# Kernel tuning notes

Measured on AMD Instinct MI355X. Metric: run time of the kernel, lower is better.

## Reference

```python
import jax, jax.numpy as jnp
import numpy as np

WIND_SIZE = 5
EPSILON = 1e-5
ALPHA = 1.0


def _windows(a, w):
    # a: [B,1,H,W] -> [B, w*w, H, W], zero-padded, window index in (di,dj) row-major
    # order matching torch's unfold(dim=2).unfold(dim=3) + reshape.
    p = w // 2
    B, _, H, W = a.shape
    ap = jnp.pad(a[:, 0], ((0, 0), (p, p), (p, p)))
    taps = [ap[:, i:i + H, j:j + W] for i in range(w) for j in range(w)]
    return jnp.stack(taps, axis=1)


def setup_inputs() -> dict:
    key = jax.random.key(0)
    ks = jax.random.split(key, 6)
    B, H, W = 4, 512, 512
    ww = WIND_SIZE * WIND_SIZE
    fake = jax.random.uniform(ks[0], (B, 1, H, W), dtype=jnp.float32)
    gamma_hdr = jax.random.uniform(ks[1], (B, 1, H, W), dtype=jnp.float32)
    # strictly positive so hdr**(1-f) is well defined
    hdr_original_im = jax.random.uniform(ks[2], (B, 1, H, W), dtype=jnp.float32) + 0.01
    r_weights = jax.random.uniform(ks[3], (B, ww, H, W), dtype=jnp.float32)
    # f_factors in [0.5, 1.5] to avoid division blow-up, realistic gamma factors
    f_factors = jax.random.uniform(ks[4], (B,), dtype=jnp.float32) + 0.5
    hdr_original_gray = jax.random.uniform(ks[5], (B, 1, H, W), dtype=jnp.float32)
    return {
        'fake': fake,
        'gamma_hdr': gamma_hdr,
        'hdr_original_im': hdr_original_im,
        'r_weights': r_weights,
        'f_factors': f_factors,
        'hdr_original_gray': hdr_original_gray,
    }


def reference(fake, gamma_hdr, hdr_original_im, r_weights, f_factors, hdr_original_gray):
    w = WIND_SIZE
    eps = jnp.float32(EPSILON)
    # create_window -> uniform window, normalized: every tap weight = 1/(w*w)
    dist_gauss = jnp.float32(1.0 / (w * w))
    weights_map = dist_gauss * r_weights                      # [B, w*w, H, W]
    weights_map_sum = jnp.sum(weights_map, axis=1, keepdims=True)  # [B,1,H,W]

    def bf_stats(x):
        xw = _windows(x, w)                                   # [B, w*w, H, W]
        mu = jnp.sum(xw * weights_map, axis=1, keepdims=True) / weights_map_sum
        var = jnp.sum((xw - mu) ** 2 * weights_map, axis=1, keepdims=True) / weights_map_sum
        std = jnp.sqrt(jnp.maximum(var, 0.0) + eps)
        return mu, std

    _, std_fake = bf_stats(fake)
    _, std_gamma = bf_stats(gamma_hdr)

    ff = f_factors[:, None, None, None]                       # [B,1,1,1]
    hdr_pow = jnp.power(hdr_original_im, 1.0 - ff)
    hw = _windows(hdr_pow, w)
    hdr_pow_mu = jnp.sum(hw * weights_map, axis=1, keepdims=True) / weights_map_sum

    w_blf = jnp.sum(r_weights, axis=1, keepdims=True) - 1.0   # [B,1,H,W]

    std_objective = (ALPHA / ff) * std_gamma * (hdr_pow_mu + eps)
    gray_max = jnp.max(hdr_original_gray.reshape(hdr_original_gray.shape[0], -1), axis=1)
    std_objective = std_objective * gray_max[:, None, None, None]

    res = 1.0 - std_fake / (std_fake + jax.lax.stop_gradient(std_objective))
    res = res * (w_blf / jnp.mean(w_blf))
    return jnp.mean(res)
```

## Files before the change

### kernel.cpp

```cpp
#include <hip/hip_runtime.h>

#define Bn 4
#define Hn 512
#define Wn 512
#define HWn (Hn * Wn)

constexpr float kEps = 1e-5f;


__global__ __launch_bounds__(256) void gmax_kernel(
    const float* __restrict__ gray, unsigned int* __restrict__ gmax_bits) {
  const int b = blockIdx.y;
  const int i = (blockIdx.x * 256 + threadIdx.x) << 2;
  const float4 g4 = *(const float4*)(gray + b * HWn + i);
  float lmax = fmaxf(fmaxf(g4.x, g4.y), fmaxf(g4.z, g4.w));
#pragma unroll
  for (int off = 32; off > 0; off >>= 1)
    lmax = fmaxf(lmax, __shfl_down(lmax, off));
  __shared__ float smax[4];
  const int lane = threadIdx.x & 63, wid = threadIdx.x >> 6;
  if (lane == 0) smax[wid] = lmax;
  __syncthreads();
  if (threadIdx.x == 0) {
    float m = fmaxf(fmaxf(smax[0], smax[1]), fmaxf(smax[2], smax[3]));
    atomicMax(&gmax_bits[b], __float_as_uint(m));
  }
}

__global__ __launch_bounds__(512, 8) void main_kernel(
    const float* __restrict__ fake, const float* __restrict__ gamma,
    const float* __restrict__ hdr, const float* __restrict__ rw,
    const float* __restrict__ ff, const unsigned int* __restrict__ gmax_bits,
    float* __restrict__ acc) {
  __shared__ float smem[3][6][512];
  __shared__ float sh1[8], sh2[8];

  const int b = blockIdx.x >> 8;
  const int h0 = (blockIdx.x & 255) << 1;
  const float e = 1.0f - ff[b];

  const float* fb = fake + (size_t)b * HWn;
  const float* gb = gamma + (size_t)b * HWn;
  const float* hb = hdr + (size_t)b * HWn;

  float4* smem4 = (float4*)smem;
#pragma unroll
  for (int k = 0; k < 5; ++k) {
    const int i = threadIdx.x + k * 512;
    if (i < 2304) {
      const int a = i / 768;
      const int rem = i - a * 768;
      const int r = rem >> 7;
      const int c4 = rem & 127;
      const int grow = min(max(h0 - 2 + r, 0), Hn - 1);
      const float* src = (a == 0) ? fb : (a == 1) ? gb : hb;
      float4 v = *(const float4*)(src + (grow << 9) + (c4 << 2));
      if (a == 2) {
        v.x = __powf(v.x, e);
        v.y = __powf(v.y, e);
        v.z = __powf(v.z, e);
        v.w = __powf(v.w, e);
      }
      smem4[i] = v;
    }
  }
  __syncthreads();

  const int p = threadIdx.x << 1;
  const int lr = p >> 9;
  const int w0 = p & (Wn - 1);
  const int h = h0 + lr;

  float Sw[2] = {0, 0}, Sf[2] = {0, 0}, Sf2[2] = {0, 0};
  float Sg[2] = {0, 0}, Sg2[2] = {0, 0}, Sh[2] = {0, 0};

  const float* rwb = rw + (size_t)b * 25 * HWn + (h << 9) + w0;

  float cm[6];
#pragma unroll
  for (int i = 0; i < 6; ++i)
    cm[i] = ((unsigned)(w0 - 2 + i) < (unsigned)Wn) ? 1.0f : 0.0f;
  const int c0 = max(w0 - 2, 0);
  const int c2 = min(w0 + 2, Wn - 2);

#pragma unroll
  for (int dyi = 0; dyi < 5; ++dyi) {
    const int r = lr + dyi;
    const float rmask = ((unsigned)(h + dyi - 2) < (unsigned)Hn) ? 1.0f : 0.0f;

    const float2 f0 = *(const float2*)&smem[0][r][c0];
    const float2 f1 = *(const float2*)&smem[0][r][w0];
    const float2 f2 = *(const float2*)&smem[0][r][c2];
    const float2 g0 = *(const float2*)&smem[1][r][c0];
    const float2 g1 = *(const float2*)&smem[1][r][w0];
    const float2 g2 = *(const float2*)&smem[1][r][c2];
    const float2 p0 = *(const float2*)&smem[2][r][c0];
    const float2 p1 = *(const float2*)&smem[2][r][w0];
    const float2 p2 = *(const float2*)&smem[2][r][c2];

    float xf[6] = {f0.x, f0.y, f1.x, f1.y, f2.x, f2.y};
    float xg[6] = {g0.x, g0.y, g1.x, g1.y, g2.x, g2.y};
    float xh[6] = {p0.x, p0.y, p1.x, p1.y, p2.x, p2.y};
#pragma unroll
    for (int i = 0; i < 6; ++i) {
      const float m = rmask * cm[i];
      xf[i] *= m;
      xg[i] *= m;
      xh[i] *= m;
    }
#pragma unroll
    for (int dxi = 0; dxi < 5; ++dxi) {
      const float2 w2 = *(const float2*)(rwb + (size_t)(dyi * 5 + dxi) * HWn);
      const float wk[2] = {w2.x, w2.y};
#pragma unroll
      for (int j = 0; j < 2; ++j) {
        const float w = wk[j];
        const float f = xf[j + dxi], g = xg[j + dxi], hp = xh[j + dxi];
        Sw[j] += w;
        Sf[j] = fmaf(w, f, Sf[j]);
        Sf2[j] = fmaf(w * f, f, Sf2[j]);
        Sg[j] = fmaf(w, g, Sg[j]);
        Sg2[j] = fmaf(w * g, g, Sg2[j]);
        Sh[j] = fmaf(w, hp, Sh[j]);
      }
    }
  }

  const float ffb = ff[b];
  const float gmax = __uint_as_float(gmax_bits[b]);
  float s1 = 0.0f, s2 = 0.0f;
#pragma unroll
  for (int j = 0; j < 2; ++j) {
    const float invSw = 1.0f / Sw[j];
    const float muf = Sf[j] * invSw;
    const float varf = fmaxf(Sf2[j] * invSw - muf * muf, 0.0f);
    const float stdf = sqrtf(varf + kEps);
    const float mug = Sg[j] * invSw;
    const float varg = fmaxf(Sg2[j] * invSw - mug * mug, 0.0f);
    const float stdg = sqrtf(varg + kEps);
    const float hpmu = Sh[j] * invSw;
    const float stdobj = (1.0f / ffb) * stdg * (hpmu + kEps) * gmax;
    const float r = 1.0f - stdf / (stdf + stdobj);
    const float wblf = Sw[j] - 1.0f;
    s1 = fmaf(r, wblf, s1);
    s2 += wblf;
  }
#pragma unroll
  for (int off = 32; off > 0; off >>= 1) {
    s1 += __shfl_down(s1, off);
    s2 += __shfl_down(s2, off);
  }
  const int lane = threadIdx.x & 63, wid = threadIdx.x >> 6;
  if (lane == 0) {
    sh1[wid] = s1;
    sh2[wid] = s2;
  }
  __syncthreads();
  if (threadIdx.x == 0) {
    float a1 = 0.0f, a2 = 0.0f;
#pragma unroll
    for (int i = 0; i < 8; ++i) {
      a1 += sh1[i];
      a2 += sh2[i];
    }
    atomicAdd(&acc[0], a1);
    atomicAdd(&acc[1], a2);
  }
}

__global__ void final_kernel(const float* __restrict__ acc,
                             float* __restrict__ out) {
  if (threadIdx.x == 0) out[0] = acc[0] / acc[1];
}

extern "C" void kernel_launch(void* const* d_in, const int* in_sizes, int n_in,
                              void* d_out, int out_size, void* d_ws,
                              size_t ws_size, hipStream_t stream) {
  const float* fake = (const float*)d_in[0];
  const float* gamma = (const float*)d_in[1];
  const float* hdr = (const float*)d_in[2];
  const float* rw = (const float*)d_in[3];
  const float* ff = (const float*)d_in[4];
  const float* gray = (const float*)d_in[5];
  float* out = (float*)d_out;
  float* ws = (float*)d_ws;
  unsigned int* gmax_bits = (unsigned int*)ws;
  float* acc = ws + 4;

  hipMemsetAsync(d_ws, 0, 64, stream);
  gmax_kernel<<<dim3(HWn / 1024, Bn), 256, 0, stream>>>(gray, gmax_bits);
  main_kernel<<<Bn * Hn / 2, 512, 0, stream>>>(fake, gamma, hdr, rw, ff,
                                               gmax_bits, acc);
  final_kernel<<<1, 64, 0, stream>>>(acc, out);
}
```

Baseline: 195.5 us.

## Process four rows and four pixels per thread with prefetched r_weights

Each block now handles four image rows instead of two and each thread computes four adjacent pixels using float4 loads. This lowers the halo overhead of the shared-memory tile (8 staged rows for 4 output rows instead of 6 for 2). The r_weights for the next window row are prefetched into registers before the shared-memory reads of the current row, to hide global-load latency. In exchange the kernel needs more registers and shared memory per block, and occupancy drops (launch bounds go from 8 to 4).

```diff
diff --git a/kernel.cpp b/kernel.cpp
--- a/kernel.cpp
+++ b/kernel.cpp
@@ -27,95 +27,109 @@
   }
 }
 
-__global__ __launch_bounds__(512, 8) void main_kernel(
+__global__ __launch_bounds__(512, 4) void main_kernel(
     const float* __restrict__ fake, const float* __restrict__ gamma,
     const float* __restrict__ hdr, const float* __restrict__ rw,
     const float* __restrict__ ff, const unsigned int* __restrict__ gmax_bits,
     float* __restrict__ acc) {
-  __shared__ float smem[3][6][512];
+  __shared__ float smem[3][8][512];
   __shared__ float sh1[8], sh2[8];
 
-  const int b = blockIdx.x >> 8;
-  const int h0 = (blockIdx.x & 255) << 1;
+  const int b = blockIdx.x >> 7;
+  const int h0 = (blockIdx.x & 127) << 2;
   const float e = 1.0f - ff[b];
 
   const float* fb = fake + (size_t)b * HWn;
   const float* gb = gamma + (size_t)b * HWn;
   const float* hb = hdr + (size_t)b * HWn;
 
+  const int t = threadIdx.x;
+  const int lr = t >> 7;
+  const int w0 = (t & 127) << 2;
+  const int h = h0 + lr;
+  const float* rwb = rw + (size_t)b * 25 * HWn + (h << 9) + w0;
+
+  float4 wv[5];
+#pragma unroll
+  for (int d = 0; d < 5; ++d)
+    wv[d] = *(const float4*)(rwb + (size_t)d * HWn);
+
   float4* smem4 = (float4*)smem;
 #pragma unroll
-  for (int k = 0; k < 5; ++k) {
-    const int i = threadIdx.x + k * 512;
-    if (i < 2304) {
-      const int a = i / 768;
-      const int rem = i - a * 768;
-      const int r = rem >> 7;
-      const int c4 = rem & 127;
-      const int grow = min(max(h0 - 2 + r, 0), Hn - 1);
-      const float* src = (a == 0) ? fb : (a == 1) ? gb : hb;
-      float4 v = *(const float4*)(src + (grow << 9) + (c4 << 2));
-      if (a == 2) {
-        v.x = __powf(v.x, e);
-        v.y = __powf(v.y, e);
-        v.z = __powf(v.z, e);
-        v.w = __powf(v.w, e);
-      }
-      smem4[i] = v;
-    }
+  for (int k = 0; k < 6; ++k) {
+    const int i = t + (k << 9);
+    const int a = i >> 10;
+    const int rem = i & 1023;
+    const int r = rem >> 7;
+    const int c4 = rem & 127;
+    const int grow = min(max(h0 - 2 + r, 0), Hn - 1);
+    const float* src = (a == 0) ? fb : (a == 1) ? gb : hb;
+    float4 v = *(const float4*)(src + (grow << 9) + (c4 << 2));
+    if (a == 2) {
+      v.x = __powf(v.x, e);
+      v.y = __powf(v.y, e);
+      v.z = __powf(v.z, e);
+      v.w = __powf(v.w, e);
+    }
+    smem4[i] = v;
   }
   __syncthreads();
 
-  const int p = threadIdx.x << 1;
-  const int lr = p >> 9;
-  const int w0 = p & (Wn - 1);
-  const int h = h0 + lr;
-
-  float Sw[2] = {0, 0}, Sf[2] = {0, 0}, Sf2[2] = {0, 0};
-  float Sg[2] = {0, 0}, Sg2[2] = {0, 0}, Sh[2] = {0, 0};
-
-  const float* rwb = rw + (size_t)b * 25 * HWn + (h << 9) + w0;
-
-  float cm[6];
-#pragma unroll
-  for (int i = 0; i < 6; ++i)
-    cm[i] = ((unsigned)(w0 - 2 + i) < (unsigned)Wn) ? 1.0f : 0.0f;
-  const int c0 = max(w0 - 2, 0);
-  const int c2 = min(w0 + 2, Wn - 2);
+  float Sw[4] = {0, 0, 0, 0}, Sf[4] = {0, 0, 0, 0}, Sf2[4] = {0, 0, 0, 0};
+  float Sg[4] = {0, 0, 0, 0}, Sg2[4] = {0, 0, 0, 0}, Sh[4] = {0, 0, 0, 0};
+
+  float cm[12];
+#pragma unroll
+  for (int i = 2; i < 10; ++i)
+    cm[i] = ((unsigned)(w0 - 4 + i) < (unsigned)Wn) ? 1.0f : 0.0f;
+  const int c0 = max(w0 - 4, 0);
+  const int c2 = min(w0 + 4, Wn - 4);
 
 #pragma unroll
   for (int dyi = 0; dyi < 5; ++dyi) {
     const int r = lr + dyi;
     const float rmask = ((unsigned)(h + dyi - 2) < (unsigned)Hn) ? 1.0f : 0.0f;
 
-    const float2 f0 = *(const float2*)&smem[0][r][c0];
-    const float2 f1 = *(const float2*)&smem[0][r][w0];
-    const float2 f2 = *(const float2*)&smem[0][r][c2];
-    const float2 g0 = *(const float2*)&smem[1][r][c0];
-    const float2 g1 = *(const float2*)&smem[1][r][w0];
-    const float2 g2 = *(const float2*)&smem[1][r][c2];
-    const float2 p0 = *(const float2*)&smem[2][r][c0];
-    const float2 p1 = *(const float2*)&smem[2][r][w0];
-    const float2 p2 = *(const float2*)&smem[2][r][c2];
-
-    float xf[6] = {f0.x, f0.y, f1.x, f1.y, f2.x, f2.y};
-    float xg[6] = {g0.x, g0.y, g1.x, g1.y, g2.x, g2.y};
-    float xh[6] = {p0.x, p0.y, p1.x, p1.y, p2.x, p2.y};
-#pragma unroll
-    for (int i = 0; i < 6; ++i) {
-      const float m = rmask * cm[i];
-      xf[i] *= m;
-      xg[i] *= m;
-      xh[i] *= m;
+    float4 wc[5];
+#pragma unroll
+    for (int d = 0; d < 5; ++d) wc[d] = wv[d];
+    if (dyi < 4) {
+#pragma unroll
+      for (int d = 0; d < 5; ++d)
+        wv[d] = *(const float4*)(rwb + (size_t)((dyi + 1) * 5 + d) * HWn);
+    }
+
+    const float4 f0 = *(const float4*)&smem[0][r][c0];
+    const float4 f1 = *(const float4*)&smem[0][r][w0];
+    const float4 f2 = *(const float4*)&smem[0][r][c2];
+    const float4 g0 = *(const float4*)&smem[1][r][c0];
+    const float4 g1 = *(const float4*)&smem[1][r][w0];
+    const float4 g2 = *(const float4*)&smem[1][r][c2];
+    const float4 p0 = *(const float4*)&smem[2][r][c0];
+    const float4 p1 = *(const float4*)&smem[2][r][w0];
+    const float4 p2 = *(const float4*)&smem[2][r][c2];
+
+    float xf[12] = {f0.x, f0.y, f0.z, f0.w, f1.x, f1.y, f1.z, f1.w,
+                    f2.x, f2.y, f2.z, f2.w};
+    float xg[12] = {g0.x, g0.y, g0.z, g0.w, g1.x, g1.y, g1.z, g1.w,
+                    g2.x, g2.y, g2.z, g2.w};
+    float xh[12] = {p0.x, p0.y, p0.z, p0.w, p1.x, p1.y, p1.z, p1.w,
+                    p2.x, p2.y, p2.z, p2.w};
+#pragma unroll
+    for (int i2 = 2; i2 < 10; ++i2) {
+      const float m = rmask * cm[i2];
+      xf[i2] *= m;
+      xg[i2] *= m;
+      xh[i2] *= m;
     }
 #pragma unroll
     for (int dxi = 0; dxi < 5; ++dxi) {
-      const float2 w2 = *(const float2*)(rwb + (size_t)(dyi * 5 + dxi) * HWn);
-      const float wk[2] = {w2.x, w2.y};
-#pragma unroll
-      for (int j = 0; j < 2; ++j) {
+      const float wk[4] = {wc[dxi].x, wc[dxi].y, wc[dxi].z, wc[dxi].w};
+#pragma unroll
+      for (int j = 0; j < 4; ++j) {
         const float w = wk[j];
-        const float f = xf[j + dxi], g = xg[j + dxi], hp = xh[j + dxi];
+        const float f = xf[j + dxi + 2], g = xg[j + dxi + 2],
+                    hp = xh[j + dxi + 2];
         Sw[j] += w;
         Sf[j] = fmaf(w, f, Sf[j]);
         Sf2[j] = fmaf(w * f, f, Sf2[j]);
@@ -130,7 +144,7 @@
   const float gmax = __uint_as_float(gmax_bits[b]);
   float s1 = 0.0f, s2 = 0.0f;
 #pragma unroll
-  for (int j = 0; j < 2; ++j) {
+  for (int j = 0; j < 4; ++j) {
     const float invSw = 1.0f / Sw[j];
     const float muf = Sf[j] * invSw;
     const float varf = fmaxf(Sf2[j] * invSw - muf * muf, 0.0f);
@@ -150,13 +164,13 @@
     s1 += __shfl_down(s1, off);
     s2 += __shfl_down(s2, off);
   }
-  const int lane = threadIdx.x & 63, wid = threadIdx.x >> 6;
+  const int lane = t & 63, wid = t >> 6;
   if (lane == 0) {
     sh1[wid] = s1;
     sh2[wid] = s2;
   }
   __syncthreads();
-  if (threadIdx.x == 0) {
+  if (t == 0) {
     float a1 = 0.0f, a2 = 0.0f;
 #pragma unroll
     for (int i = 0; i < 8; ++i) {
@@ -189,7 +203,7 @@
 
   hipMemsetAsync(d_ws, 0, 64, stream);
   gmax_kernel<<<dim3(HWn / 1024, Bn), 256, 0, stream>>>(gray, gmax_bits);
-  main_kernel<<<Bn * Hn / 2, 512, 0, stream>>>(fake, gamma, hdr, rw, ff,
+  main_kernel<<<Bn * Hn / 4, 512, 0, stream>>>(fake, gamma, hdr, rw, ff,
                                                gmax_bits, acc);
   final_kernel<<<1, 64, 0, stream>>>(acc, out);
 }
```

Result: faster. 190.1 us (-2.8%).
